# Performance work log

Hardware: AMD Instinct MI355X
Metric: run time of the kernel (lower is better)

## Reference

```python
import jax, jax.numpy as jnp
import numpy as np

B = 4096      # graphs per batch
V = 32        # vertices per graph
F = 16        # num_atom_types (input node features)
NB = 8        # num_bond_types (edge feature dim)
C = 128       # conv_dim
E_PER = 256   # random edges per graph
NEG_SLOPE = 0.2


def setup_inputs() -> dict:
    rng = np.random.default_rng(0)
    N = B * V
    # random intra-graph edges (duplicates are fine; softmax handles them)
    off = (np.arange(B, dtype=np.int64) * V)[:, None]
    src = (rng.integers(0, V, (B, E_PER)) + off).ravel()
    dst = (rng.integers(0, V, (B, E_PER)) + off).ravel()
    bond = rng.integers(0, NB, src.shape[0])
    eattr = np.zeros((src.shape[0], NB), dtype=np.float32)
    eattr[np.arange(src.shape[0]), bond] = 1.0
    # self loops with edge_attr = per-target-node mean (PyG fill_value='mean')
    sums = np.zeros((N, NB), dtype=np.float64)
    np.add.at(sums, dst, eattr)
    cnt = np.bincount(dst, minlength=N).astype(np.float64)
    loop_attr = (sums / np.maximum(cnt, 1.0)[:, None]).astype(np.float32)
    loops = np.arange(N, dtype=np.int64)
    edge_index = np.stack([np.concatenate([src, loops]),
                           np.concatenate([dst, loops])])  # [2, E]
    edge_attr = np.concatenate([eattr, loop_attr], axis=0)  # [E, NB]

    key = jax.random.key(0)
    ks = jax.random.split(key, 8)
    inp = {
        "x": jax.random.normal(ks[0], (N, F), jnp.float32),
        "edge_index": jnp.asarray(edge_index),
        "edge_attr": jnp.asarray(edge_attr),
        "W_lin": jax.random.normal(ks[1], (F, C), jnp.float32) / np.sqrt(F),
        "att_src": jax.random.normal(ks[2], (C,), jnp.float32) / np.sqrt(C),
        "att_dst": jax.random.normal(ks[3], (C,), jnp.float32) / np.sqrt(C),
        "att_edge": jax.random.normal(ks[4], (C,), jnp.float32) / np.sqrt(C),
        "W_edge": jax.random.normal(ks[5], (NB, C), jnp.float32) / np.sqrt(NB),
        "b_gat": jnp.zeros((C,), jnp.float32),
        "W_out": jax.random.normal(ks[6], (C, 1), jnp.float32) / np.sqrt(C),
        "b_out": jnp.zeros((1,), jnp.float32),
        "num_graphs": B,
    }
    return inp


def reference(x, edge_index, edge_attr, W_lin, att_src, att_dst, att_edge,
              W_edge, b_gat, W_out, b_out, num_graphs):
    N = x.shape[0]
    src, dst = edge_index[0], edge_index[1]
    h = x @ W_lin                           # [N, C] node transform
    a_src = h @ att_src                     # [N]
    a_dst = h @ att_dst                     # [N]
    a_edge = (edge_attr @ W_edge) @ att_edge  # [E]
    alpha = jax.nn.leaky_relu(a_src[src] + a_dst[dst] + a_edge, NEG_SLOPE)
    # segment softmax over incoming edges of each dst node
    m = jax.ops.segment_max(alpha, dst, num_segments=N)
    m = jnp.where(jnp.isfinite(m), m, 0.0)
    ex = jnp.exp(alpha - m[dst])
    denom = jax.ops.segment_sum(ex, dst, num_segments=N)
    w = ex / denom[dst]                     # [E] attention weights
    msg = h[src] * w[:, None]               # [E, C]
    out_nodes = jax.ops.segment_sum(msg, dst, num_segments=N) + b_gat  # [N, C]
    gf = out_nodes.reshape(num_graphs, -1, out_nodes.shape[-1]).mean(axis=1)  # [B, C]
    out = gf @ W_out + b_out                # [B, 1]
    return (out, gf)
```

## Files before the change

### kernel.cpp

```cpp
#include <hip/hip_runtime.h>


#define BB   4096
#define VV   32
#define FF   16
#define NBB  8
#define CC   128
#define EPER 256
constexpr int NTOT  = BB * VV;
constexpr int ERAND = BB * EPER;
constexpr int ETOT  = ERAND + NTOT;
constexpr float SLOPE = 0.2f;

__launch_bounds__(256, 4)
__global__ void gnn_all(const float* __restrict__ x,
                        const int*   __restrict__ eidx,
                        const float* __restrict__ eattr,
                        const float* __restrict__ W_lin,
                        const float* __restrict__ att_src,
                        const float* __restrict__ att_dst,
                        const float* __restrict__ att_edge,
                        const float* __restrict__ W_edge,
                        const float* __restrict__ b_gat,
                        const float* __restrict__ W_out,
                        const float* __restrict__ b_out,
                        float* __restrict__ out,
                        float* __restrict__ gf_out)
{
  const int t    = threadIdx.x;
  const int lane = t & 63;
  const int wave = __builtin_amdgcn_readfirstlane(t) >> 6;
  const int g    = blockIdx.x * 4 + wave;
  const int half = lane >> 5;
  const int v    = lane & 31;

  __shared__ float2 s_a[4][VV];
  __shared__ float  s_den[4][VV];
  __shared__ float  s_r[4][VV];
  __shared__ float2 s_uv[4][FF];
  __shared__ __align__(16) float s_we[4][NBB];
  __shared__ float  s_xt[4][FF * 33];
  __shared__ __align__(16) float s_y[4][FF];

  float4 xa, xb;
  {
    const float* xp = x + (size_t)(g * VV + v) * FF + half * 8;
    xa = ((const float4*)xp)[0]; xb = ((const float4*)xp)[1];
  }
  int es[4], ed[4];
  float4 ea0[4], ea1[4];
  #pragma unroll
  for (int k = 0; k < 4; ++k) {
    const int e = g * EPER + 64 * k + lane;
    es[k] = eidx[e] - g * VV;
    ed[k] = eidx[ETOT + e] - g * VV;
    const float4* ap = (const float4*)(eattr + (size_t)e * NBB);
    ea0[k] = ap[0]; ea1[k] = ap[1];
  }
  float4 la0 = {0,0,0,0}, la1 = {0,0,0,0};
  if (half) {
    const float4* lp = (const float4*)(eattr + (size_t)(ERAND + g * VV + v) * NBB);
    la0 = lp[0]; la1 = lp[1];
  }

  {
    const int fu = lane & 15, q = lane >> 4;
    const float4* wr = (const float4*)(W_lin + fu * CC + q * 32);
    const float4* as = (const float4*)(att_src + q * 32);
    const float4* ad = (const float4*)(att_dst + q * 32);
    float us = 0.f, ud = 0.f;
    #pragma unroll
    for (int j = 0; j < 8; ++j) {
      const float4 w = wr[j], a = as[j], d = ad[j];
      us += w.x*a.x + w.y*a.y + w.z*a.z + w.w*a.w;
      ud += w.x*d.x + w.y*d.y + w.z*d.z + w.w*d.w;
    }
    us += __shfl_xor(us, 16); us += __shfl_xor(us, 32);
    ud += __shfl_xor(ud, 16); ud += __shfl_xor(ud, 32);
    if (lane < FF) s_uv[wave][lane] = make_float2(us, ud);
  }
  if (!half) {
    const int f8 = v & 7, oct = v >> 3;
    const float4* wr = (const float4*)(W_edge + f8 * CC + oct * 32);
    const float4* ae = (const float4*)(att_edge + oct * 32);
    float pe = 0.f;
    #pragma unroll
    for (int j = 0; j < 8; ++j) {
      const float4 w = wr[j], a = ae[j];
      pe += w.x*a.x + w.y*a.y + w.z*a.z + w.w*a.w;
    }
    pe += __shfl_xor(pe, 8); pe += __shfl_xor(pe, 16);
    if (v < NBB) s_we[wave][v] = pe;
  }

  float a0 = 0.f, a1 = 0.f;
  {
    const float xr[8] = {xa.x, xa.y, xa.z, xa.w, xb.x, xb.y, xb.z, xb.w};
    #pragma unroll
    for (int j = 0; j < 8; ++j) {
      const float2 u = s_uv[wave][half * 8 + j];
      a0 += xr[j] * u.x; a1 += xr[j] * u.y;
    }
  }
  a0 += __shfl_xor(a0, 32); a1 += __shfl_xor(a1, 32);
  if (!half) {
    s_a[wave][v] = make_float2(a0, a1);
    s_den[wave][v] = 0.f; s_r[wave][v] = 0.f;
  }
  __threadfence_block();

  const float4 w03 = *(const float4*)&s_we[wave][0];
  const float4 w47 = *(const float4*)&s_we[wave][4];
  float ex[5];
  #pragma unroll
  for (int k = 0; k < 4; ++k) {
    const float2 A = s_a[wave][es[k]];
    const float2 D = s_a[wave][ed[k]];
    const float aed = ea0[k].x*w03.x + ea0[k].y*w03.y + ea0[k].z*w03.z + ea0[k].w*w03.w
                    + ea1[k].x*w47.x + ea1[k].y*w47.y + ea1[k].z*w47.z + ea1[k].w*w47.w;
    const float a  = A.x + D.y + aed;
    const float al = a > 0.f ? a : SLOPE * a;
    ex[k] = __expf(al);
    atomicAdd(&s_den[wave][ed[k]], ex[k]);
  }
  ex[4] = 0.f;
  if (half) {
    const float2 S = s_a[wave][v];
    const float aed = la0.x*w03.x + la0.y*w03.y + la0.z*w03.z + la0.w*w03.w
                    + la1.x*w47.x + la1.y*w47.y + la1.z*w47.z + la1.w*w47.w;
    const float a  = S.x + S.y + aed;
    const float al = a > 0.f ? a : SLOPE * a;
    ex[4] = __expf(al);
    atomicAdd(&s_den[wave][v], ex[4]);
  }
  __threadfence_block();

  #pragma unroll
  for (int k = 0; k < 4; ++k)
    atomicAdd(&s_r[wave][es[k]], ex[k] * __builtin_amdgcn_rcpf(s_den[wave][ed[k]]));
  if (half)
    atomicAdd(&s_r[wave][v], ex[4] * __builtin_amdgcn_rcpf(s_den[wave][v]));
  __threadfence_block();

  {
    const float rl = s_r[wave][v];
    const float xr[8] = {xa.x, xa.y, xa.z, xa.w, xb.x, xb.y, xb.z, xb.w};
    #pragma unroll
    for (int j = 0; j < 8; ++j)
      s_xt[wave][(half * 8 + j) * 33 + v] = xr[j] * rl;
  }
  __threadfence_block();
  {
    const int fy = lane & 15, part = lane >> 4;
    float yp = 0.f;
    #pragma unroll
    for (int j = 0; j < 8; ++j) yp += s_xt[wave][fy * 33 + part * 8 + j];
    yp += __shfl_xor(yp, 16); yp += __shfl_xor(yp, 32);
    if (lane < FF) s_y[wave][lane] = yp * (1.0f / VV);
  }
  __threadfence_block();

  const float4 y03 = *(const float4*)&s_y[wave][0];
  const float4 y47 = *(const float4*)&s_y[wave][4];
  const float4 y8b = *(const float4*)&s_y[wave][8];
  const float4 ycf = *(const float4*)&s_y[wave][12];
  const float yv[16] = {y03.x,y03.y,y03.z,y03.w, y47.x,y47.y,y47.z,y47.w,
                        y8b.x,y8b.y,y8b.z,y8b.w, ycf.x,ycf.y,ycf.z,ycf.w};
  const float2 bg = ((const float2*)b_gat)[lane];
  float gx = bg.x, gy = bg.y;
  const float2* W2 = (const float2*)W_lin;
  #pragma unroll
  for (int f = 0; f < FF; ++f) {
    const float2 w = W2[f * 64 + lane];
    gx += yv[f] * w.x; gy += yv[f] * w.y;
  }
  ((float2*)(gf_out + (size_t)g * CC))[lane] = make_float2(gx, gy);

  const float2 wo = ((const float2*)W_out)[lane];
  float p = gx * wo.x + gy * wo.y;
  #pragma unroll
  for (int m = 1; m <= 32; m <<= 1) p += __shfl_xor(p, m);
  if (lane == 0) out[g] = p + b_out[0];
}

extern "C" void kernel_launch(void* const* d_in, const int* in_sizes, int n_in,
                              void* d_out, int out_size, void* d_ws, size_t ws_size,
                              hipStream_t stream) {
  const float* x        = (const float*)d_in[0];
  const int*   eidx     = (const int*)  d_in[1];
  const float* eattr    = (const float*)d_in[2];
  const float* W_lin    = (const float*)d_in[3];
  const float* att_src  = (const float*)d_in[4];
  const float* att_dst  = (const float*)d_in[5];
  const float* att_edge = (const float*)d_in[6];
  const float* W_edge   = (const float*)d_in[7];
  const float* b_gat    = (const float*)d_in[8];
  const float* W_out    = (const float*)d_in[9];
  const float* b_out    = (const float*)d_in[10];

  float* out = (float*)d_out;
  float* gf  = out + BB;

  gnn_all<<<dim3(BB / 4), dim3(256), 0, stream>>>(
      x, eidx, eattr, W_lin, att_src, att_dst, att_edge, W_edge,
      b_gat, W_out, b_out, out, gf);
}
```

Baseline: 117.5 us.

## Map one graph per 128-thread block instead of one graph per wave

Work is redistributed so each graph is handled by a full 128-thread block (two waves) instead of a single 64-lane wave, launching 4096 small blocks. Per-thread edge work halves, and the node projection, weight-vector precompute and final GEMV are re-split across more threads. Wave-local fences become block-wide __syncthreads, with an extra cross-wave reduction through shared memory for the output dot. The kernel is latency-bound, so the goal is more parallelism per graph and lower per-thread serial latency, at the cost of barrier overhead and more blocks.

```diff
diff --git a/kernel.cpp b/kernel.cpp
--- a/kernel.cpp
+++ b/kernel.cpp
@@ -7,12 +7,11 @@
 #define NBB  8
 #define CC   128
 #define EPER 256
-constexpr int NTOT  = BB * VV;
 constexpr int ERAND = BB * EPER;
-constexpr int ETOT  = ERAND + NTOT;
+constexpr int ETOT  = ERAND + BB * VV;
 constexpr float SLOPE = 0.2f;
 
-__launch_bounds__(256, 4)
+__launch_bounds__(128, 8)
 __global__ void gnn_all(const float* __restrict__ x,
                         const int*   __restrict__ eidx,
                         const float* __restrict__ eattr,
@@ -29,41 +28,40 @@
 {
   const int t    = threadIdx.x;
   const int lane = t & 63;
-  const int wave = __builtin_amdgcn_readfirstlane(t) >> 6;
-  const int g    = blockIdx.x * 4 + wave;
-  const int half = lane >> 5;
-  const int v    = lane & 31;
-
-  __shared__ float2 s_a[4][VV];
-  __shared__ float  s_den[4][VV];
-  __shared__ float  s_r[4][VV];
-  __shared__ float2 s_uv[4][FF];
-  __shared__ __align__(16) float s_we[4][NBB];
-  __shared__ float  s_xt[4][FF * 33];
-  __shared__ __align__(16) float s_y[4][FF];
-
-  float4 xa, xb;
-  {
-    const float* xp = x + (size_t)(g * VV + v) * FF + half * 8;
-    xa = ((const float4*)xp)[0]; xb = ((const float4*)xp)[1];
-  }
-  int es[4], ed[4];
-  float4 ea0[4], ea1[4];
-  #pragma unroll
-  for (int k = 0; k < 4; ++k) {
-    const int e = g * EPER + 64 * k + lane;
+  const int g    = blockIdx.x;
+  const int row  = t >> 2;
+  const int q4   = t & 3;
+
+  __shared__ float2 s_a[VV];
+  __shared__ float  s_den[VV], s_r[VV];
+  __shared__ float2 s_uv[FF];
+  __shared__ __align__(16) float s_we[NBB];
+  __shared__ float  s_xt[FF * 33];
+  __shared__ __align__(16) float s_y[FF];
+  __shared__ float  s_p[2];
+
+  if (t < VV) { s_den[t] = 0.f; s_r[t] = 0.f; }
+  if (t < FF) s_y[t] = 0.f;
+
+  const float4 xv = ((const float4*)(x + (size_t)(g * VV + row) * FF))[q4];
+
+  int es[2], ed[2];
+  float4 ea0[2], ea1[2];
+  #pragma unroll
+  for (int k = 0; k < 2; ++k) {
+    const int e = g * EPER + 128 * k + t;
     es[k] = eidx[e] - g * VV;
     ed[k] = eidx[ETOT + e] - g * VV;
     const float4* ap = (const float4*)(eattr + (size_t)e * NBB);
     ea0[k] = ap[0]; ea1[k] = ap[1];
   }
   float4 la0 = {0,0,0,0}, la1 = {0,0,0,0};
-  if (half) {
-    const float4* lp = (const float4*)(eattr + (size_t)(ERAND + g * VV + v) * NBB);
+  if (t >= 96) {
+    const float4* lp = (const float4*)(eattr + (size_t)(ERAND + g * VV + (t - 96)) * NBB);
     la0 = lp[0]; la1 = lp[1];
   }
 
-  {
+  if (t < 64) {
     const int fu = lane & 15, q = lane >> 4;
     const float4* wr = (const float4*)(W_lin + fu * CC + q * 32);
     const float4* as = (const float4*)(att_src + q * 32);
@@ -77,110 +75,108 @@
     }
     us += __shfl_xor(us, 16); us += __shfl_xor(us, 32);
     ud += __shfl_xor(ud, 16); ud += __shfl_xor(ud, 32);
-    if (lane < FF) s_uv[wave][lane] = make_float2(us, ud);
-  }
-  if (!half) {
-    const int f8 = v & 7, oct = v >> 3;
-    const float4* wr = (const float4*)(W_edge + f8 * CC + oct * 32);
-    const float4* ae = (const float4*)(att_edge + oct * 32);
+    if (lane < FF) s_uv[lane] = make_float2(us, ud);
+  } else {
+    const int f8 = lane & 7, oct = lane >> 3;
+    const float4* wr = (const float4*)(W_edge + f8 * CC + oct * 16);
+    const float4* ae = (const float4*)(att_edge + oct * 16);
     float pe = 0.f;
     #pragma unroll
-    for (int j = 0; j < 8; ++j) {
+    for (int j = 0; j < 4; ++j) {
       const float4 w = wr[j], a = ae[j];
       pe += w.x*a.x + w.y*a.y + w.z*a.z + w.w*a.w;
     }
-    pe += __shfl_xor(pe, 8); pe += __shfl_xor(pe, 16);
-    if (v < NBB) s_we[wave][v] = pe;
-  }
-
-  float a0 = 0.f, a1 = 0.f;
+    pe += __shfl_xor(pe, 8); pe += __shfl_xor(pe, 16); pe += __shfl_xor(pe, 32);
+    if (lane < NBB) s_we[lane] = pe;
+  }
+  __syncthreads();
+
   {
-    const float xr[8] = {xa.x, xa.y, xa.z, xa.w, xb.x, xb.y, xb.z, xb.w};
-    #pragma unroll
-    for (int j = 0; j < 8; ++j) {
-      const float2 u = s_uv[wave][half * 8 + j];
-      a0 += xr[j] * u.x; a1 += xr[j] * u.y;
+    const float xf[4] = {xv.x, xv.y, xv.z, xv.w};
+    float a0 = 0.f, a1 = 0.f;
+    #pragma unroll
+    for (int j = 0; j < 4; ++j) {
+      const float2 u = s_uv[q4 * 4 + j];
+      a0 += xf[j] * u.x; a1 += xf[j] * u.y;
     }
-  }
-  a0 += __shfl_xor(a0, 32); a1 += __shfl_xor(a1, 32);
-  if (!half) {
-    s_a[wave][v] = make_float2(a0, a1);
-    s_den[wave][v] = 0.f; s_r[wave][v] = 0.f;
-  }
-  __threadfence_block();
-
-  const float4 w03 = *(const float4*)&s_we[wave][0];
-  const float4 w47 = *(const float4*)&s_we[wave][4];
-  float ex[5];
-  #pragma unroll
-  for (int k = 0; k < 4; ++k) {
-    const float2 A = s_a[wave][es[k]];
-    const float2 D = s_a[wave][ed[k]];
+    a0 += __shfl_xor(a0, 1); a0 += __shfl_xor(a0, 2);
+    a1 += __shfl_xor(a1, 1); a1 += __shfl_xor(a1, 2);
+    if (q4 == 0) s_a[row] = make_float2(a0, a1);
+  }
+  __syncthreads();
+
+  const float4 w03 = *(const float4*)&s_we[0];
+  const float4 w47 = *(const float4*)&s_we[4];
+  float ex[3];
+  #pragma unroll
+  for (int k = 0; k < 2; ++k) {
+    const float2 A = s_a[es[k]];
+    const float2 D = s_a[ed[k]];
     const float aed = ea0[k].x*w03.x + ea0[k].y*w03.y + ea0[k].z*w03.z + ea0[k].w*w03.w
                     + ea1[k].x*w47.x + ea1[k].y*w47.y + ea1[k].z*w47.z + ea1[k].w*w47.w;
     const float a  = A.x + D.y + aed;
     const float al = a > 0.f ? a : SLOPE * a;
     ex[k] = __expf(al);
-    atomicAdd(&s_den[wave][ed[k]], ex[k]);
-  }
-  ex[4] = 0.f;
-  if (half) {
-    const float2 S = s_a[wave][v];
+    atomicAdd(&s_den[ed[k]], ex[k]);
+  }
+  ex[2] = 0.f;
+  if (t >= 96) {
+    const int v = t - 96;
+    const float2 S = s_a[v];
     const float aed = la0.x*w03.x + la0.y*w03.y + la0.z*w03.z + la0.w*w03.w
                     + la1.x*w47.x + la1.y*w47.y + la1.z*w47.z + la1.w*w47.w;
     const float a  = S.x + S.y + aed;
     const float al = a > 0.f ? a : SLOPE * a;
-    ex[4] = __expf(al);
-    atomicAdd(&s_den[wave][v], ex[4]);
-  }
-  __threadfence_block();
-
-  #pragma unroll
-  for (int k = 0; k < 4; ++k)
-    atomicAdd(&s_r[wave][es[k]], ex[k] * __builtin_amdgcn_rcpf(s_den[wave][ed[k]]));
-  if (half)
-    atomicAdd(&s_r[wave][v], ex[4] * __builtin_amdgcn_rcpf(s_den[wave][v]));
-  __threadfence_block();
+    ex[2] = __expf(al);
+    atomicAdd(&s_den[v], ex[2]);
+  }
+  __syncthreads();
+
+  #pragma unroll
+  for (int k = 0; k < 2; ++k)
+    atomicAdd(&s_r[es[k]], ex[k] * __builtin_amdgcn_rcpf(s_den[ed[k]]));
+  if (t >= 96) {
+    const int v = t - 96;
+    atomicAdd(&s_r[v], ex[2] * __builtin_amdgcn_rcpf(s_den[v]));
+  }
+  __syncthreads();
 
   {
-    const float rl = s_r[wave][v];
-    const float xr[8] = {xa.x, xa.y, xa.z, xa.w, xb.x, xb.y, xb.z, xb.w};
-    #pragma unroll
-    for (int j = 0; j < 8; ++j)
-      s_xt[wave][(half * 8 + j) * 33 + v] = xr[j] * rl;
-  }
-  __threadfence_block();
+    const float rl = s_r[row];
+    const float xf[4] = {xv.x, xv.y, xv.z, xv.w};
+    #pragma unroll
+    for (int j = 0; j < 4; ++j)
+      s_xt[(q4 * 4 + j) * 33 + row] = xf[j] * rl;
+  }
+  __syncthreads();
   {
-    const int fy = lane & 15, part = lane >> 4;
+    const int f = t & 15, part = t >> 4;
     float yp = 0.f;
     #pragma unroll
-    for (int j = 0; j < 8; ++j) yp += s_xt[wave][fy * 33 + part * 8 + j];
+    for (int j = 0; j < 4; ++j) yp += s_xt[f * 33 + part * 4 + j];
     yp += __shfl_xor(yp, 16); yp += __shfl_xor(yp, 32);
-    if (lane < FF) s_y[wave][lane] = yp * (1.0f / VV);
-  }
-  __threadfence_block();
-
-  const float4 y03 = *(const float4*)&s_y[wave][0];
-  const float4 y47 = *(const float4*)&s_y[wave][4];
-  const float4 y8b = *(const float4*)&s_y[wave][8];
-  const float4 ycf = *(const float4*)&s_y[wave][12];
+    if (lane < FF) atomicAdd(&s_y[lane], yp);
+  }
+  __syncthreads();
+
+  const float4 y03 = *(const float4*)&s_y[0];
+  const float4 y47 = *(const float4*)&s_y[4];
+  const float4 y8b = *(const float4*)&s_y[8];
+  const float4 ycf = *(const float4*)&s_y[12];
   const float yv[16] = {y03.x,y03.y,y03.z,y03.w, y47.x,y47.y,y47.z,y47.w,
                         y8b.x,y8b.y,y8b.z,y8b.w, ycf.x,ycf.y,ycf.z,ycf.w};
-  const float2 bg = ((const float2*)b_gat)[lane];
-  float gx = bg.x, gy = bg.y;
-  const float2* W2 = (const float2*)W_lin;
-  #pragma unroll
-  for (int f = 0; f < FF; ++f) {
-    const float2 w = W2[f * 64 + lane];
-    gx += yv[f] * w.x; gy += yv[f] * w.y;
-  }
-  ((float2*)(gf_out + (size_t)g * CC))[lane] = make_float2(gx, gy);
-
-  const float2 wo = ((const float2*)W_out)[lane];
-  float p = gx * wo.x + gy * wo.y;
+  float gx = b_gat[t];
+  #pragma unroll
+  for (int f = 0; f < FF; ++f)
+    gx += (yv[f] * (1.0f / VV)) * W_lin[f * CC + t];
+  gf_out[(size_t)g * CC + t] = gx;
+
+  float p = gx * W_out[t];
   #pragma unroll
   for (int m = 1; m <= 32; m <<= 1) p += __shfl_xor(p, m);
-  if (lane == 0) out[g] = p + b_out[0];
+  if (lane == 0) s_p[t >> 6] = p;
+  __syncthreads();
+  if (t == 0) out[g] = s_p[0] + s_p[1] + b_out[0];
 }
 
 extern "C" void kernel_launch(void* const* d_in, const int* in_sizes, int n_in,
@@ -201,7 +197,7 @@
   float* out = (float*)d_out;
   float* gf  = out + BB;
 
-  gnn_all<<<dim3(BB / 4), dim3(256), 0, stream>>>(
+  gnn_all<<<dim3(BB), dim3(128), 0, stream>>>(
       x, eidx, eattr, W_lin, att_src, att_dst, att_edge, W_edge,
       b_gat, W_out, b_out, out, gf);
 }
```

After: 136.3 us. +16.0%, slower.
